# Kernel optimization log

Measured on AMD Instinct MI355X. Metric: run time of the kernel, lower is better.

The kernel has to match this reference:

```python
import jax, jax.numpy as jnp
import numpy as np
from jax import lax

# Dense-equivalent of the spconv net: SubMConv/SparseConv with stride 1 and
# size-preserving padding on a dense input reduce to ordinary conv2d.
# Layer chain: (1->64,k1) PReLU (64->256,k3) PReLU (256->512,k3) PReLU
# (512->256,k3) PReLU (256->64,k3) PReLU (64->1,k3) PReLU, then symmetrize.

CHANS = [(1, 64, 1), (64, 256, 3), (256, 512, 3), (512, 256, 3), (256, 64, 3), (64, 1, 3)]


def _conv(x, w, b, k):
    pad = ((k // 2, k // 2), (k // 2, k // 2))
    y = lax.conv_general_dilated(x, w, window_strides=(1, 1), padding=pad,
                                 dimension_numbers=('NCHW', 'OIHW', 'NCHW'))
    return y + b[None, :, None, None]


def _prelu(x, a):
    return jnp.where(x >= 0, x, a * x)


def setup_inputs() -> dict:
    key = jax.random.key(0)
    keys = jax.random.split(key, 1 + 2 * len(CHANS))
    inp = {'A': jax.random.normal(keys[0], (1, 1, 512, 512), dtype=jnp.float32)}
    for i, (cin, cout, k) in enumerate(CHANS):
        fan_in = cin * k * k
        std = 1.0 / np.sqrt(fan_in)
        inp[f'w{i}'] = jax.random.normal(keys[1 + 2 * i], (cout, cin, k, k), dtype=jnp.float32) * std
        inp[f'b{i}'] = jax.random.normal(keys[2 + 2 * i], (cout,), dtype=jnp.float32) * std
        inp[f'p{i}'] = jnp.full((1,), 0.25, dtype=jnp.float32)  # PReLU default weight
    return inp


def reference(A, w0, b0, p0, w1, b1, p1, w2, b2, p2, w3, b3, p3, w4, b4, p4, w5, b5, p5):
    params = [(w0, b0, p0), (w1, b1, p1), (w2, b2, p2), (w3, b3, p3), (w4, b4, p4), (w5, b5, p5)]
    x = A
    for (w, b, p), (_, _, k) in zip(params, CHANS):
        x = _prelu(_conv(x, w, b, k), p)
    # make_symmetric: average with transpose over the spatial (matrix) dims
    return 0.5 * (x + jnp.swapaxes(x, -1, -2))
```

## Files before the change

kernel.cpp:

```cpp
#include <hip/hip_runtime.h>
#include <hip/hip_bf16.h>
#include <stdint.h>

typedef __bf16 bf16_t;
typedef __bf16 bf16x8 __attribute__((ext_vector_type(8)));
typedef float  f32x4  __attribute__((ext_vector_type(4)));

#define HP 514
#define AS1 __attribute__((address_space(1)))
#define AS3 __attribute__((address_space(3)))

__device__ __forceinline__ bf16_t f2bf(float f) { return (bf16_t)f; }

__global__ void l0_kernel(const float* __restrict__ A, const float* __restrict__ w0,
                          const float* __restrict__ b0, const float* __restrict__ p0,
                          bf16_t* __restrict__ X0)
{
    int idx = blockIdx.x * 256 + threadIdx.x;
    if (idx >= HP * HP * 64) return;
    int c   = idx & 63;
    int pix = idx >> 6;
    int py = pix / HP, px = pix - py * HP;
    float v = 0.f;
    if (py >= 1 && py <= 512 && px >= 1 && px <= 512) {
        float a = A[(py - 1) * 512 + (px - 1)];
        v = fmaf(w0[c], a, b0[c]);
        v = v >= 0.f ? v : p0[0] * v;
    }
    X0[idx] = f2bf(v);
}

__global__ void zero_rows_kernel(bf16_t* __restrict__ buf, int C, int r0, int n)
{
    int idx = blockIdx.x * 256 + threadIdx.x;
    int rowsz = HP * C;
    if (idx >= n * rowsz) return;
    int r = idx / rowsz, j = idx - r * rowsz;
    buf[(size_t)(r0 + r) * rowsz + j] = f2bf(0.f);
}

__global__ void zero_cols_kernel(bf16_t* __restrict__ buf, int C, int R)
{
    int idx = blockIdx.x * 256 + threadIdx.x;
    if (idx >= R * 2 * C) return;
    int r = idx / (2 * C);
    int t = idx - r * 2 * C;
    int col = (t < C) ? 0 : 513;
    int c = t % C;
    buf[((size_t)r * HP + col) * C + c] = f2bf(0.f);
}

__global__ void wtrans_kernel(const float* __restrict__ w, bf16_t* __restrict__ wt,
                              int COUT, int CIN)
{
    int idx = blockIdx.x * 256 + threadIdx.x;
    if (idx >= COUT * CIN * 9) return;
    int G    = COUT / 16;
    int j    = idx & 7;
    int l    = (idx >> 3) & 63;
    int t    = idx >> 9;
    int gabs = t % G;
    int t2   = t / G;
    int tap  = t2 % 9;
    int ci   = t2 / 9;
    int cout = gabs * 16 + (l & 15);
    int cin  = ci * 32 + (l >> 4) * 8 + j;
    wt[idx] = f2bf(w[(cout * CIN + cin) * 9 + tap]);
}

template<int CIN, int COUT, int BN>
__global__ __launch_bounds__(256, 3)
void conv3x3_kernel(const bf16_t* __restrict__ in, const bf16_t* __restrict__ wt,
                    const float* __restrict__ bias, const float* __restrict__ alpha,
                    bf16_t* __restrict__ out,
                    int n_rows, int in_off, int in_alloc, int out_off)
{
    constexpr int G      = COUT / 16;
    constexpr int NT     = BN / 32;
    constexpr int NC     = CIN / 32;
    constexpr int AUNITS = 18 * 10 * 4;
    constexpr int APAD   = 768;
    constexpr int ASLAB  = APAD * 8;
    constexpr int ROWB   = BN * 2;
    constexpr int SMASK  = ROWB / 32 - 1;
    constexpr int SMEM_B = (4 * ASLAB * 2 > 128 * ROWB) ? 4 * ASLAB * 2 : 128 * ROWB;
    __shared__ __align__(16) char smem[SMEM_B];
    bf16_t* As = (bf16_t*)smem;

    const int tid  = threadIdx.x;
    const int lane = tid & 63;
    const int wave = tid >> 6;
    const int lm   = lane & 15;
    const int quad = lane >> 4;
    const int wave_m = wave >> 1;
    const int wave_n = wave & 1;

    const int bid  = blockIdx.x + 64 * (blockIdx.y + gridDim.y * blockIdx.z);
    const int nwg  = 64 * gridDim.y * gridDim.z;
    const int sid  = (bid & 7) * (nwg >> 3) + (bid >> 3);
    const int zsh  = __ffs(gridDim.z) - 1;
    const int szb  = sid & (gridDim.z - 1);
    const int t2   = sid >> zsh;
    const int sx   = t2 & 63;
    const int syb  = t2 >> 6;

    const int x0 = sx * 8;
    const int y0 = syb * 16;
    const int zb = szb;
    const int gb_blk = zb * (BN / 16);

    int a_srcb[3];
    #pragma unroll
    for (int it = 0; it < 3; ++it) {
        int u  = it * 256 + tid;
        int uu = u < AUNITS ? u : AUNITS - 1;
        int qq = uu & 3, px = (uu >> 2) % 10, r = uu / 40;
        int q  = (qq - (px >> 1)) & 3;
        int grow = in_off + y0 + r;
        grow = grow < 0 ? 0 : (grow >= in_alloc ? in_alloc - 1 : grow);
        a_srcb[it] = (grow * HP + x0 + px) * CIN + q * 8;
    }

    const int pxb = lm & 7, pyb = lm >> 3;
    int sw[3];
    #pragma unroll
    for (int dx = 0; dx < 3; ++dx)
        sw[dx] = ((quad + ((pxb + dx) >> 1)) & 3) * 8;
    int addrA0[4];
    #pragma unroll
    for (int mt = 0; mt < 4; ++mt)
        addrA0[mt] = ((wave_m * 8 + mt * 2 + pyb) * 40 + pxb * 4) * 8;

    auto stageA = [&](int cc, int base) {
        #pragma unroll
        for (int it = 0; it < 3; ++it) {
            const bf16_t* src = in + a_srcb[it] + cc;
            bf16_t* dst = As + base + (it * 256 + wave * 64) * 8;
            __builtin_amdgcn_global_load_lds((AS1 void*)src, (AS3 void*)dst, 16, 0, 0);
        }
    };
    auto loadB = [&](int ft, bf16x8* b) {
        const bf16_t* base = wt + ((size_t)ft * G + gb_blk + wave_n * NT) * 512 + lane * 8;
        #pragma unroll
        for (int nt = 0; nt < NT; ++nt)
            b[nt] = *(const bf16x8*)(base + nt * 512);
    };
    auto readA = [&](int base, int tap, bf16x8* a) {
        const int dy = tap / 3, dx = tap - dy * 3;
        const int shift = (dy * 40 + dx * 4) * 8 + sw[dx];
        #pragma unroll
        for (int mt = 0; mt < 4; ++mt)
            a[mt] = *(const bf16x8*)(As + base + addrA0[mt] + shift);
    };

    f32x4 acc[4][NT] = {};
    bf16x8 breg[2][NT];
    bf16x8 areg[2][4];

    stageA(0, 0);
    stageA(32, ASLAB);
    loadB(0, breg[0]);
    __syncthreads();
    readA(0, 0, areg[0]);

    for (int cp = 0; cp < NC / 2; ++cp) {
        const bool morecp = (cp + 1 < NC / 2);
        const int fb  = cp * 18;
        const int sb0 = ((2 * cp)     & 3) * ASLAB;
        const int sb1 = ((2 * cp + 1) & 3) * ASLAB;
        const int sb2 = ((2 * cp + 2) & 3) * ASLAB;
        const int sb3 = ((2 * cp + 3) & 3) * ASLAB;
        #pragma unroll
        for (int rf = 0; rf < 18; ++rf) {
            if (rf < 17 || morecp)
                loadB(fb + rf + 1, breg[(rf + 1) & 1]);
            if (rf == 0 && 2 * cp + 2 < NC) stageA((2 * cp + 2) * 32, sb2);
            if (rf == 9 && 2 * cp + 3 < NC) stageA((2 * cp + 3) * 32, sb3);
            if (rf <= 7)        readA(sb0, rf + 1, areg[(rf + 1) & 1]);
            else if (rf == 8)   readA(sb1, 0, areg[1]);
            else if (rf <= 16)  readA(sb1, rf - 8, areg[(rf + 1) & 1]);
            else if (morecp)    readA(sb2, 0, areg[0]);

            __builtin_amdgcn_s_setprio(1);
            #pragma unroll
            for (int mt = 0; mt < 4; ++mt)
                #pragma unroll
                for (int nt = 0; nt < NT; ++nt)
                    acc[mt][nt] = __builtin_amdgcn_mfma_f32_16x16x32_bf16(
                        areg[rf & 1][mt], breg[rf & 1][nt], acc[mt][nt], 0, 0, 0);
            __builtin_amdgcn_s_setprio(0);

            if (rf == 8)             __syncthreads();
            if (rf == 17 && morecp)  __syncthreads();
        }
    }

    __syncthreads();
    const float al = alpha[0];
    #pragma unroll
    for (int nt = 0; nt < NT; ++nt) {
        const int c  = wave_n * (BN / 2) + nt * 16 + lm;
        const float bv = bias[zb * BN + c];
        #pragma unroll
        for (int mt = 0; mt < 4; ++mt) {
            f32x4 v = acc[mt][nt];
            #pragma unroll
            for (int r = 0; r < 4; ++r) {
                int m = wave_m * 64 + mt * 16 + quad * 4 + r;
                float f = v[r] + bv;
                f = f >= 0.f ? f : al * f;
                int byte = m * ROWB + ((c * 2) ^ ((m & SMASK) << 5));
                *(bf16_t*)(smem + byte) = f2bf(f);
            }
        }
    }
    __syncthreads();
    constexpr int CPI  = ROWB / 16;
    constexpr int ITER = (128 * CPI) / 256;
    #pragma unroll
    for (int i = 0; i < ITER; ++i) {
        int g = i * 256 + tid;
        int p = g / CPI;
        int k = g & (CPI - 1);
        int sbyte = p * ROWB + ((k * 16) ^ ((p & SMASK) << 5));
        bf16x8 v16 = *(const bf16x8*)(smem + sbyte);
        int py = p >> 3, px = p & 7, ly = y0 + py;
        if (ly < n_rows)
            *(bf16x8*)(out + ((size_t)(out_off + ly) * HP + (x0 + px + 1)) * COUT
                       + zb * BN + k * 8) = v16;
    }
}

__device__ __forceinline__ float conv64_at(const bf16_t* __restrict__ X,
                                           const float* __restrict__ wsh,
                                           int y, int x, float bv)
{
    float acc = bv;
    #pragma unroll
    for (int dy = 0; dy < 3; ++dy) {
        #pragma unroll
        for (int dx = 0; dx < 3; ++dx) {
            const bf16x8* p = (const bf16x8*)(X + ((size_t)(y + dy) * HP + (x + dx)) * 64);
            const float* wf = wsh + (dy * 3 + dx) * 64;
            #pragma unroll
            for (int j = 0; j < 8; ++j) {
                bf16x8 v = p[j];
                #pragma unroll
                for (int k = 0; k < 8; ++k)
                    acc = fmaf((float)v[k], wf[j * 8 + k], acc);
            }
        }
    }
    return acc;
}

__global__ __launch_bounds__(256)
void l5_strip_kernel(const bf16_t* __restrict__ B4, const bf16_t* __restrict__ wt5,
                     const float* __restrict__ b5, const float* __restrict__ p5,
                     float* __restrict__ T, int abs_row0)
{
    __shared__ float wsh[9 * 64];
    for (int i = threadIdx.x; i < 576; i += 256) wsh[i] = (float)wt5[i];
    __syncthreads();
    int idx = blockIdx.x * 256 + threadIdx.x;
    int ly = idx >> 9, x = idx & 511;
    float bv = b5[0], al = p5[0];
    float t = conv64_at(B4, wsh, ly, x, bv);
    t = t >= 0.f ? t : al * t;
    T[(size_t)(abs_row0 + ly) * 512 + x] = t;
}

__global__ void wtrans5_kernel(const float* __restrict__ w, bf16_t* __restrict__ wt)
{
    int idx = blockIdx.x * 256 + threadIdx.x;
    if (idx >= 9 * 64) return;
    int cin = idx % 64, tap = idx / 64;
    wt[idx] = f2bf(w[cin * 9 + tap]);
}

__global__ __launch_bounds__(256)
void sym_kernel(const float* __restrict__ T, float* __restrict__ out)
{
    int idx = blockIdx.x * 256 + threadIdx.x;
    int y = idx >> 9, x = idx & 511;
    out[idx] = 0.5f * (T[idx] + T[x * 512 + y]);
}

extern "C" void kernel_launch(void* const* d_in, const int* in_sizes, int n_in,
                              void* d_out, int out_size, void* d_ws, size_t ws_size,
                              hipStream_t stream)
{
    const float* A = (const float*)d_in[0];
    const float *w[6], *b[6], *p[6];
    for (int i = 0; i < 6; ++i) {
        w[i] = (const float*)d_in[1 + 3 * i];
        b[i] = (const float*)d_in[2 + 3 * i];
        p[i] = (const float*)d_in[3 + 3 * i];
    }

    auto footprint = [](long long S) -> size_t {
        auto al = [](size_t v) { return (v + 255) & ~(size_t)255; };
        size_t t = 0;
        t += al((size_t)HP * HP * 64 * 2);
        t += al((size_t)(S + 8) * HP * 256 * 2);
        t += al((size_t)(S + 6) * HP * 512 * 2);
        t += al((size_t)(S + 2) * HP * 64 * 2);
        t += al((size_t)512 * 512 * 4);
        t += al((size_t)9 * 256 * 64 * 2);
        t += al((size_t)9 * 512 * 256 * 2);
        t += al((size_t)9 * 256 * 512 * 2);
        t += al((size_t)9 * 64 * 256 * 2);
        t += al((size_t)9 * 64 * 2);
        return t;
    };
    const int cand[6] = {512, 256, 128, 64, 32, 16};
    int S = 16;
    for (int i = 0; i < 6; ++i)
        if (footprint(cand[i]) <= ws_size) { S = cand[i]; break; }
    const int nStrips = 512 / S;

    char* ws = (char*)d_ws;
    size_t off = 0;
    auto carve = [&](size_t bytes) -> void* {
        void* r = ws + off;
        off += (bytes + 255) & ~(size_t)255;
        return r;
    };
    bf16_t* X0  = (bf16_t*)carve((size_t)HP * HP * 64 * 2);
    bf16_t* B1  = (bf16_t*)carve((size_t)(S + 8) * HP * 256 * 2);
    bf16_t* B2  = (bf16_t*)carve((size_t)(S + 6) * HP * 512 * 2);
    bf16_t* B4  = (bf16_t*)carve((size_t)(S + 2) * HP * 64 * 2);
    float*  T   = (float*)carve((size_t)512 * 512 * 4);
    bf16_t* wt1 = (bf16_t*)carve((size_t)9 * 256 * 64 * 2);
    bf16_t* wt2 = (bf16_t*)carve((size_t)9 * 512 * 256 * 2);
    bf16_t* wt3 = (bf16_t*)carve((size_t)9 * 256 * 512 * 2);
    bf16_t* wt4 = (bf16_t*)carve((size_t)9 * 64 * 256 * 2);
    bf16_t* wt5 = (bf16_t*)carve((size_t)9 * 64 * 2);
    bf16_t* B3  = B1;

    auto cdiv = [](int a, int bq) { return (a + bq - 1) / bq; };
    auto zrows = [&](bf16_t* buf, int C, int r0, int n) {
        if (n > 0)
            zero_rows_kernel<<<cdiv(n * HP * C, 256), 256, 0, stream>>>(buf, C, r0, n);
    };

    wtrans_kernel<<<cdiv(9 * 256 * 64, 256), 256, 0, stream>>>(w[1], wt1, 256, 64);
    wtrans_kernel<<<cdiv(9 * 512 * 256, 256), 256, 0, stream>>>(w[2], wt2, 512, 256);
    wtrans_kernel<<<cdiv(9 * 256 * 512, 256), 256, 0, stream>>>(w[3], wt3, 256, 512);
    wtrans_kernel<<<cdiv(9 * 64 * 256, 256), 256, 0, stream>>>(w[4], wt4, 64, 256);
    wtrans5_kernel<<<cdiv(9 * 64, 256), 256, 0, stream>>>(w[5], wt5);
    l0_kernel<<<cdiv(HP * HP * 64, 256), 256, 0, stream>>>(A, w[0], b[0], p[0], X0);
    zero_cols_kernel<<<cdiv((S + 8) * 2 * 256, 256), 256, 0, stream>>>(B1, 256, S + 8);
    zero_cols_kernel<<<cdiv((S + 6) * 2 * 512, 256), 256, 0, stream>>>(B2, 512, S + 6);
    zero_cols_kernel<<<cdiv((S + 2) * 2 * 64, 256), 256, 0, stream>>>(B4, 64, S + 2);

    for (int s = 0; s < nStrips; ++s) {
        const int base = S * s;
        int o0[5], nn[5], ooff[5], alloc[5];
        for (int k = 1; k <= 4; ++k) {
            int hk = 5 - k;
            int a0 = base - hk, a1 = base + S + hk;
            int c0 = a0 < 0 ? 0 : a0, c1 = a1 > 512 ? 512 : a1;
            o0[k] = c0; nn[k] = c1 - c0; ooff[k] = c0 - a0; alloc[k] = S + 2 * hk;
        }
        {
            int in_off = o0[1];
            dim3 g(64, cdiv(nn[1], 16), 2);
            conv3x3_kernel<64, 256, 128><<<g, 256, 0, stream>>>(
                X0, wt1, b[1], p[1], B1, nn[1], in_off, 514, ooff[1]);
            zrows(B1, 256, 0, ooff[1]);
            zrows(B1, 256, ooff[1] + nn[1], alloc[1] - ooff[1] - nn[1]);
        }
        {
            int in_off = (o0[2] - 1) - (base - 4);
            dim3 g(64, cdiv(nn[2], 16), 4);
            conv3x3_kernel<256, 512, 128><<<g, 256, 0, stream>>>(
                B1, wt2, b[2], p[2], B2, nn[2], in_off, alloc[1], ooff[2]);
            zrows(B2, 512, 0, ooff[2]);
            zrows(B2, 512, ooff[2] + nn[2], alloc[2] - ooff[2] - nn[2]);
        }
        {
            int in_off = (o0[3] - 1) - (base - 3);
            dim3 g(64, cdiv(nn[3], 16), 2);
            conv3x3_kernel<512, 256, 128><<<g, 256, 0, stream>>>(
                B2, wt3, b[3], p[3], B3, nn[3], in_off, alloc[2], ooff[3]);
            zrows(B3, 256, 0, ooff[3]);
            zrows(B3, 256, ooff[3] + nn[3], alloc[3] - ooff[3] - nn[3]);
        }
        {
            int in_off = (o0[4] - 1) - (base - 2);
            dim3 g(64, cdiv(nn[4], 16), 1);
            conv3x3_kernel<256, 64, 64><<<g, 256, 0, stream>>>(
                B3, wt4, b[4], p[4], B4, nn[4], in_off, alloc[3], ooff[4]);
            zrows(B4, 64, 0, ooff[4]);
            zrows(B4, 64, ooff[4] + nn[4], alloc[4] - ooff[4] - nn[4]);
        }
        l5_strip_kernel<<<(S * 512) / 256, 256, 0, stream>>>(B4, wt5, b[5], p[5], T, base);
    }

    sym_kernel<<<(512 * 512) / 256, 256, 0, stream>>>(T, (float*)d_out);
}
```

Before: 1.384 ms.

## Switch conv3x3 MFMA from 16x16x32 to 32x32x16 bf16 tiles

Replaces the 16x16x32 bf16 MFMA tiling in the implicit-GEMM 3x3 conv with 32x32x16 MFMAs. Each 32-channel chunk is split into two K-halves, and the weight pre-transpose layout, LDS read addressing and swizzle, and epilogue row mapping are changed to match. The larger MFMA tile needs fewer A/B register fragments per FLOP and is meant to cut LDS and global operand traffic per MFMA. The cost is heavier accumulator register use and new swizzle index arithmetic that must be correct.

```diff
diff --git a/kernel.cpp b/kernel.cpp
--- a/kernel.cpp
+++ b/kernel.cpp
@@ -5,6 +5,7 @@
 typedef __bf16 bf16_t;
 typedef __bf16 bf16x8 __attribute__((ext_vector_type(8)));
 typedef float  f32x4  __attribute__((ext_vector_type(4)));
+typedef float  f32x16 __attribute__((ext_vector_type(16)));
 
 #define HP 514
 #define AS1 __attribute__((address_space(1)))
@@ -55,16 +56,18 @@
 {
     int idx = blockIdx.x * 256 + threadIdx.x;
     if (idx >= COUT * CIN * 9) return;
-    int G    = COUT / 16;
+    int G32  = COUT / 32;
     int j    = idx & 7;
     int l    = (idx >> 3) & 63;
     int t    = idx >> 9;
-    int gabs = t % G;
-    int t2   = t / G;
-    int tap  = t2 % 9;
-    int ci   = t2 / 9;
-    int cout = gabs * 16 + (l & 15);
-    int cin  = ci * 32 + (l >> 4) * 8 + j;
+    int g    = t % G32;
+    int t2   = t / G32;
+    int ks   = t2 & 1;
+    int t3   = t2 >> 1;
+    int tap  = t3 % 9;
+    int chunk= t3 / 9;
+    int cout = g * 32 + (l & 31);
+    int cin  = chunk * 32 + ks * 16 + (l >> 5) * 8 + j;
     wt[idx] = f2bf(w[(cout * CIN + cin) * 9 + tap]);
 }
 
@@ -75,8 +78,8 @@
                     bf16_t* __restrict__ out,
                     int n_rows, int in_off, int in_alloc, int out_off)
 {
-    constexpr int G      = COUT / 16;
-    constexpr int NT     = BN / 32;
+    constexpr int G32    = COUT / 32;
+    constexpr int NTF    = BN / 64;
     constexpr int NC     = CIN / 32;
     constexpr int AUNITS = 18 * 10 * 4;
     constexpr int APAD   = 768;
@@ -90,8 +93,8 @@
     const int tid  = threadIdx.x;
     const int lane = tid & 63;
     const int wave = tid >> 6;
-    const int lm   = lane & 15;
-    const int quad = lane >> 4;
+    const int l31  = lane & 31;
+    const int half = lane >> 5;
     const int wave_m = wave >> 1;
     const int wave_n = wave & 1;
 
@@ -107,7 +110,7 @@
     const int x0 = sx * 8;
     const int y0 = syb * 16;
     const int zb = szb;
-    const int gb_blk = zb * (BN / 16);
+    const int gb_blk = zb * (BN / 32);
 
     int a_srcb[3];
     #pragma unroll
@@ -121,15 +124,18 @@
         a_srcb[it] = (grow * HP + x0 + px) * CIN + q * 8;
     }
 
-    const int pxb = lm & 7, pyb = lm >> 3;
-    int sw[3];
-    #pragma unroll
-    for (int dx = 0; dx < 3; ++dx)
-        sw[dx] = ((quad + ((pxb + dx) >> 1)) & 3) * 8;
-    int addrA0[4];
-    #pragma unroll
-    for (int mt = 0; mt < 4; ++mt)
-        addrA0[mt] = ((wave_m * 8 + mt * 2 + pyb) * 40 + pxb * 4) * 8;
+    const int pxb  = lane & 7;
+    const int rpart = l31 >> 3;
+    int sw32[2][3];
+    #pragma unroll
+    for (int ks = 0; ks < 2; ++ks)
+        #pragma unroll
+        for (int dx = 0; dx < 3; ++dx)
+            sw32[ks][dx] = ((ks * 2 + half + ((pxb + dx) >> 1)) & 3) * 8;
+    int addrA0[2];
+    #pragma unroll
+    for (int mt = 0; mt < 2; ++mt)
+        addrA0[mt] = ((wave_m * 8 + mt * 4 + rpart) * 40 + pxb * 4) * 8;
 
     auto stageA = [&](int cc, int base) {
         #pragma unroll
@@ -139,23 +145,29 @@
             __builtin_amdgcn_global_load_lds((AS1 void*)src, (AS3 void*)dst, 16, 0, 0);
         }
     };
-    auto loadB = [&](int ft, bf16x8* b) {
-        const bf16_t* base = wt + ((size_t)ft * G + gb_blk + wave_n * NT) * 512 + lane * 8;
-        #pragma unroll
-        for (int nt = 0; nt < NT; ++nt)
-            b[nt] = *(const bf16x8*)(base + nt * 512);
-    };
-    auto readA = [&](int base, int tap, bf16x8* a) {
+    auto loadB = [&](int ft, bf16x8 (&b)[NTF][2]) {
+        #pragma unroll
+        for (int nt = 0; nt < NTF; ++nt)
+            #pragma unroll
+            for (int ks = 0; ks < 2; ++ks) {
+                const int g = gb_blk + wave_n * NTF + nt;
+                const bf16_t* base = wt + (((size_t)ft * 2 + ks) * G32 + g) * 512 + lane * 8;
+                b[nt][ks] = *(const bf16x8*)(base);
+            }
+    };
+    auto readA = [&](int base, int tap, bf16x8 (&a)[2][2]) {
         const int dy = tap / 3, dx = tap - dy * 3;
-        const int shift = (dy * 40 + dx * 4) * 8 + sw[dx];
-        #pragma unroll
-        for (int mt = 0; mt < 4; ++mt)
-            a[mt] = *(const bf16x8*)(As + base + addrA0[mt] + shift);
-    };
-
-    f32x4 acc[4][NT] = {};
-    bf16x8 breg[2][NT];
-    bf16x8 areg[2][4];
+        #pragma unroll
+        for (int mt = 0; mt < 2; ++mt)
+            #pragma unroll
+            for (int ks = 0; ks < 2; ++ks)
+                a[mt][ks] = *(const bf16x8*)(As + base + addrA0[mt]
+                                             + (dy * 40 + dx * 4) * 8 + sw32[ks][dx]);
+    };
+
+    f32x16 acc[2][NTF] = {};
+    bf16x8 breg[2][NTF][2];
+    bf16x8 areg[2][2][2];
 
     stageA(0, 0);
     stageA(32, ASLAB);
@@ -183,11 +195,14 @@
 
             __builtin_amdgcn_s_setprio(1);
             #pragma unroll
-            for (int mt = 0; mt < 4; ++mt)
+            for (int mt = 0; mt < 2; ++mt)
                 #pragma unroll
-                for (int nt = 0; nt < NT; ++nt)
-                    acc[mt][nt] = __builtin_amdgcn_mfma_f32_16x16x32_bf16(
-                        areg[rf & 1][mt], breg[rf & 1][nt], acc[mt][nt], 0, 0, 0);
+                for (int nt = 0; nt < NTF; ++nt) {
+                    acc[mt][nt] = __builtin_amdgcn_mfma_f32_32x32x16_bf16(
+                        areg[rf & 1][mt][0], breg[rf & 1][nt][0], acc[mt][nt], 0, 0, 0);
+                    acc[mt][nt] = __builtin_amdgcn_mfma_f32_32x32x16_bf16(
+                        areg[rf & 1][mt][1], breg[rf & 1][nt][1], acc[mt][nt], 0, 0, 0);
+                }
             __builtin_amdgcn_s_setprio(0);
 
             if (rf == 8)             __syncthreads();
@@ -198,16 +213,16 @@
     __syncthreads();
     const float al = alpha[0];
     #pragma unroll
-    for (int nt = 0; nt < NT; ++nt) {
-        const int c  = wave_n * (BN / 2) + nt * 16 + lm;
+    for (int nt = 0; nt < NTF; ++nt) {
+        const int c  = wave_n * (BN / 2) + nt * 32 + l31;
         const float bv = bias[zb * BN + c];
         #pragma unroll
-        for (int mt = 0; mt < 4; ++mt) {
-            f32x4 v = acc[mt][nt];
+        for (int mt = 0; mt < 2; ++mt) {
+            f32x16 v = acc[mt][nt];
             #pragma unroll
-            for (int r = 0; r < 4; ++r) {
-                int m = wave_m * 64 + mt * 16 + quad * 4 + r;
-                float f = v[r] + bv;
+            for (int i = 0; i < 16; ++i) {
+                int m = wave_m * 64 + mt * 32 + (i & 3) + 8 * (i >> 2) + 4 * half;
+                float f = v[i] + bv;
                 f = f >= 0.f ? f : al * f;
                 int byte = m * ROWB + ((c * 2) ^ ((m & SMASK) << 5));
                 *(bf16_t*)(smem + byte) = f2bf(f);
```

After: 1.647 ms. +19.0%, slower.
